# Performance work log

Hardware: AMD Instinct MI355X
Metric: run time of the kernel (lower is better)

Reference implementation:

```python
import jax, jax.numpy as jnp
import numpy as np

L, B, E = 2048, 4, 1024
H = 8
D1 = 2048          # expand_ratio * E, multiple of H
HD = D1 // H       # head dim 256
MAX_L = 2048
EPS = 1e-8


def setup_inputs() -> dict:
    key = jax.random.key(0)
    ks = jax.random.split(key, 9)
    std = 0.02
    return {
        "x": jax.random.normal(ks[0], (L, B, E), jnp.float32),
        "Wu": jax.random.normal(ks[1], (D1, E), jnp.float32) * std,
        "bu": jax.random.normal(ks[2], (D1,), jnp.float32) * std,
        "Wv": jax.random.normal(ks[3], (D1, E), jnp.float32) * std,
        "bv": jax.random.normal(ks[4], (D1,), jnp.float32) * std,
        "Wo": jax.random.normal(ks[5], (E, D1), jnp.float32) * std,
        "bo": jax.random.normal(ks[6], (E,), jnp.float32) * std,
        "zero": jax.random.normal(ks[7], (H, 1), jnp.float32) * 0.1,   # Toeplitz coef, offset 0
        "pos": jax.random.normal(ks[8], (H, MAX_L - 1), jnp.float32) * 0.1,  # offsets 1..n-1
    }


def _simple_rmsnorm(x):
    d = x.shape[-1]
    rms = jnp.linalg.norm(x, axis=-1, keepdims=True) * (d ** -0.5)
    return x / (rms + EPS)


def _toeplitz_causal_fft(v, zero, pos):
    # v: (b, h, n, hd); causal Toeplitz mixing along n via FFT long conv
    n = v.shape[-2]
    coef = jnp.concatenate([zero, pos[:, : n - 1]], axis=-1)  # (h, n)
    m = 2 * n
    cf = jnp.fft.rfft(coef, m, axis=-1)                  # (h, m//2+1)
    vf = jnp.fft.rfft(v, m, axis=-2)                     # (b, h, m//2+1, hd)
    out = jnp.fft.irfft(cf[None, :, :, None] * vf, m, axis=-2)
    return out[:, :, :n, :]


def reference(x, Wu, bu, Wv, bv, Wo, bo, zero, pos):
    # x: (n, b, e) fairseq layout
    n, b, e = x.shape
    shortcut = x
    xn = _simple_rmsnorm(x)                               # pre_norm (SimpleRMSNorm, no params)
    u = jax.nn.silu(jnp.einsum('nbe,de->nbd', xn, Wu) + bu)   # (n,b,d1)
    v = jax.nn.silu(jnp.einsum('nbe,de->nbd', xn, Wv) + bv)   # (n,b,d1)
    # 'n b (h d) -> b h n d'
    vh = v.transpose(1, 0, 2).reshape(b, n, H, HD).transpose(0, 2, 1, 3)
    oh = _toeplitz_causal_fft(vh, zero, pos)              # (b,h,n,hd)
    o = oh.transpose(0, 2, 1, 3).reshape(b, n, D1).transpose(1, 0, 2)  # (n,b,d1)
    o = u * o                                             # gating
    out = jnp.einsum('nbd,ed->nbe', o, Wo) + bo + shortcut
    return out
```

## Files before the change

kernel.cpp:

```cpp
#include <hip/hip_runtime.h>
#include <cstdint>
#include <cstddef>

#define LQ   2048
#define BQ   4
#define EQ   1024
#define HQ   8
#define D1Q  2048
#define HDQ  256
#define NBQ  (LQ*BQ)

typedef __bf16 bf16_t;
typedef __bf16 bf16x8 __attribute__((ext_vector_type(8)));
typedef __bf16 bf16x4 __attribute__((ext_vector_type(4)));
typedef float  f32x4  __attribute__((ext_vector_type(4)));

#define GAS1(p) ((const __attribute__((address_space(1))) void*)(p))
#define LAS3(p) ((__attribute__((address_space(3))) void*)(p))


__global__ __launch_bounds__(256) void convert_kernel(
    const float* __restrict__ Wu, const float* __restrict__ Wv,
    const float* __restrict__ Wo,
    bf16_t* __restrict__ Wub, bf16_t* __restrict__ Wvb,
    bf16_t* __restrict__ Wob)
{
    const size_t i = ((size_t)blockIdx.x * 256 + threadIdx.x) * 4;
    if (i < (size_t)D1Q * EQ) {
        float4 a = *(const float4*)(Wu + i);
        float4 b = *(const float4*)(Wv + i);
        float4 d = *(const float4*)(Wo + i);
        bf16x4 oa, ob, od;
        oa[0]=(bf16_t)a.x; oa[1]=(bf16_t)a.y; oa[2]=(bf16_t)a.z; oa[3]=(bf16_t)a.w;
        ob[0]=(bf16_t)b.x; ob[1]=(bf16_t)b.y; ob[2]=(bf16_t)b.z; ob[3]=(bf16_t)b.w;
        od[0]=(bf16_t)d.x; od[1]=(bf16_t)d.y; od[2]=(bf16_t)d.z; od[3]=(bf16_t)d.w;
        *(bf16x4*)(Wub + i) = oa;
        *(bf16x4*)(Wvb + i) = ob;
        *(bf16x4*)(Wob + i) = od;
    }
}

__global__ __launch_bounds__(256) void build_toep_tiles(
    const float* __restrict__ zero, const float* __restrict__ pos,
    bf16_t* __restrict__ Atiles)
{
    const int q = blockIdx.x;
    const int h = blockIdx.y;
    const int doff = (q - 3) * 32;
    const int tid = threadIdx.x;
    bf16_t* dst = Atiles + ((size_t)h * 64 + q) * (128 * 32);
    const int e0 = tid * 16;
    const int r = e0 >> 5;
    const int cbase = e0 & 31;
    bf16_t vals[16];
    #pragma unroll
    for (int j = 0; j < 16; ++j) {
        const int d = doff + r - (cbase + j);
        float v = 0.f;
        if (d == 0) v = zero[h];
        else if (d > 0) v = pos[(size_t)h * (LQ - 1) + d - 1];
        vals[j] = (bf16_t)v;
    }
    *(bf16x8*)(dst + e0)     = *(bf16x8*)(vals);
    *(bf16x8*)(dst + e0 + 8) = *(bf16x8*)(vals + 8);
}

__global__ __launch_bounds__(256) void rmsnorm_kernel(
    const float* __restrict__ x, bf16_t* __restrict__ xn)
{
    const int row = blockIdx.x;
    const int tid = threadIdx.x;
    const float4 v = ((const float4*)(x + (size_t)row * EQ))[tid];
    float ss = v.x*v.x + v.y*v.y + v.z*v.z + v.w*v.w;
    #pragma unroll
    for (int m = 32; m >= 1; m >>= 1) ss += __shfl_xor(ss, m, 64);
    __shared__ float red[4];
    const int wid = tid >> 6, lane = tid & 63;
    if (lane == 0) red[wid] = ss;
    __syncthreads();
    const float tot = red[0] + red[1] + red[2] + red[3];
    const float inv = 1.f / (sqrtf(tot * (1.f / EQ)) + 1e-8f);
    bf16x4 o;
    o[0] = (bf16_t)(v.x * inv); o[1] = (bf16_t)(v.y * inv);
    o[2] = (bf16_t)(v.z * inv); o[3] = (bf16_t)(v.w * inv);
    *(bf16x4*)(xn + (size_t)row * EQ + tid * 4) = o;
}


__global__ __launch_bounds__(512, 2) void gemm_uv(
    const bf16_t* __restrict__ A, const bf16_t* __restrict__ Bm,
    const float* __restrict__ bbu, const float* __restrict__ bbv,
    bf16_t* __restrict__ Ub, bf16_t* __restrict__ Vt)
{
    constexpr int K = EQ;
    constexpr int BUF = 24576;
    __shared__ alignas(16) char smem[3 * BUF];

    const int nwg   = gridDim.x * gridDim.y;
    const int bid0  = blockIdx.y * gridDim.x + blockIdx.x;
    const int chunkw = nwg >> 3;
    const int sb    = (bid0 & 7) * chunkw + (bid0 >> 3);
    const int bx    = sb % gridDim.x;
    const int by    = sb / gridDim.x;

    const int tid  = threadIdx.x;
    const int wid  = tid >> 6;
    const int lane = tid & 63;
    const int frow = lane & 15;
    const int c    = lane >> 4;
    const int m0 = by * 256;
    const int n0 = bx * 128;
    const int wm = wid >> 1, wn = wid & 1;
    const int wrm = wm * 64, wrn = wn * 64;

    const int g = (frow >> 1) & 3;
    const int offA0 = (wrm + frow) * 64 + ((c ^ g) << 4);
    const int offB0 = 16384 + (wrn + frow) * 64 + ((c ^ g) << 4);

    const int rA   = tid >> 2;
    const int soff = (((tid & 3) ^ ((rA >> 1) & 3)) << 4);
    const size_t lda2 = (size_t)K * 2;
    const char* sA = (const char*)A  + (size_t)(m0 + rA) * lda2 + soff;
    const char* sB = (const char*)Bm + (size_t)(n0 + rA) * lda2 + soff;

    auto STAGE = [&](int bf, int kt) {
        char* dA = smem + bf * BUF + wid * 1024;
        __builtin_amdgcn_global_load_lds(GAS1(sA + (size_t)kt * 64), LAS3(dA), 16, 0, 0);
        __builtin_amdgcn_global_load_lds(GAS1(sA + 128 * lda2 + (size_t)kt * 64),
                                         LAS3(dA + 8192), 16, 0, 0);
        char* dB = smem + bf * BUF + 16384 + wid * 1024;
        __builtin_amdgcn_global_load_lds(GAS1(sB + (size_t)kt * 64), LAS3(dB), 16, 0, 0);
    };

    f32x4 acc[4][4];
    #pragma unroll
    for (int i = 0; i < 4; ++i)
        #pragma unroll
        for (int j = 0; j < 4; ++j) acc[i][j] = (f32x4){0.f, 0.f, 0.f, 0.f};

    const int NT = K >> 5;

    STAGE(0, 0); STAGE(1, 1);
    asm volatile("s_waitcnt vmcnt(3)" ::: "memory");
    __builtin_amdgcn_s_barrier();

    int cur = 0, pb = 2;
    for (int t = 0; t < NT; ++t) {
        if (t + 2 < NT) STAGE(pb, t + 2);
        const char* base = smem + cur * BUF;
        bf16x8 av[4], bv[4];
        #pragma unroll
        for (int i = 0; i < 4; ++i) {
            av[i] = *(const bf16x8*)(base + offA0 + i * 1024);
            bv[i] = *(const bf16x8*)(base + offB0 + i * 1024);
        }
        __builtin_amdgcn_s_setprio(1);
        #pragma unroll
        for (int mi = 0; mi < 4; ++mi)
            #pragma unroll
            for (int ni = 0; ni < 4; ++ni)
                acc[mi][ni] = __builtin_amdgcn_mfma_f32_16x16x32_bf16(
                    av[mi], bv[ni], acc[mi][ni], 0, 0, 0);
        __builtin_amdgcn_s_setprio(0);
        if (t + 1 < NT) {
            if (t + 2 < NT) asm volatile("s_waitcnt vmcnt(3)" ::: "memory");
            else            asm volatile("s_waitcnt vmcnt(0)" ::: "memory");
            __builtin_amdgcn_s_barrier();
        }
        cur = (cur == 2) ? 0 : cur + 1;
        pb  = (pb  == 2) ? 0 : pb  + 1;
    }

    if (bx < 16) {
        const int fq = c * 4;
        #pragma unroll
        for (int mi = 0; mi < 4; ++mi) {
            #pragma unroll
            for (int ni = 0; ni < 4; ++ni) {
                const int gn = n0 + wrn + ni * 16 + frow;
                #pragma unroll
                for (int j = 0; j < 4; ++j) {
                    const int gm = m0 + wrm + mi * 16 + fq + j;
                    float v = acc[mi][ni][j] + bbu[gn];
                    v = v / (1.f + __expf(-v));
                    Ub[(size_t)gm * D1Q + gn] = (bf16_t)v;
                }
            }
        }
        return;
    }

    {
        const int n0v = n0 - 2048;
        const int hh  = n0v >> 8;
        const int hdb = (n0v & 255) + wrn;
        float bb[4];
        #pragma unroll
        for (int ni = 0; ni < 4; ++ni) bb[ni] = bbv[n0v + wrn + ni * 16 + frow];

        bf16_t* chunk = (bf16_t*)smem + wn * 8448;
        #pragma unroll
        for (int p = 0; p < 2; ++p) {
            __syncthreads();
            #pragma unroll
            for (int mi = 0; mi < 4; ++mi) {
                #pragma unroll
                for (int nio = 0; nio < 2; ++nio) {
                    const int ni = p * 2 + nio;
                    const int nl = nio * 16 + frow;
                    const int tl = wm * 16 + mi * 4 + c;
                    #pragma unroll
                    for (int j = 0; j < 4; ++j) {
                        float v = acc[mi][ni][j] + bb[ni];
                        v = v / (1.f + __expf(-v));
                        chunk[nl * 264 + j * 64 + tl] = (bf16_t)v;
                    }
                }
            }
            __syncthreads();
            const int nl    = lane & 31;
            const int thalf = lane >> 5;
            const int b2    = wm;
            const int hd    = hdb + p * 32 + nl;
            const int t0    = (m0 >> 2) + thalf * 32;
            const bf16_t* src = chunk + nl * 264 + b2 * 64 + thalf * 32;
            bf16_t* dst = Vt + (((size_t)hh * 4 + b2) * 256 + hd) * (size_t)LQ + t0;
            #pragma unroll
            for (int u = 0; u < 4; ++u)
                *(bf16x8*)(dst + u * 8) = *(const bf16x8*)(src + u * 8);
        }
    }
}

__global__ __launch_bounds__(512, 2) void gemm_toep(
    const bf16_t* __restrict__ VT, const bf16_t* __restrict__ Atiles,
    const bf16_t* __restrict__ U, bf16_t* __restrict__ O)
{
    constexpr int BUF = 24576;
    __shared__ alignas(16) char smem[3 * BUF];

    const int bid   = blockIdx.x;
    const int m_blk = 15 - (bid >> 5);
    const int sub   = bid & 31;
    const int h     = sub >> 2;
    const int n0    = (sub & 3) * 256;
    const int m0    = m_blk * 128;

    const int tid  = threadIdx.x;
    const int wid  = tid >> 6;
    const int lane = tid & 63;
    const int frow = lane & 15;
    const int c    = lane >> 4;
    const int wrm  = (wid >> 2) * 64;
    const int wrn  = (wid & 3) * 64;

    const int g = (frow >> 1) & 3;
    const int offA0 = (wrm + frow) * 64 + ((c ^ g) << 4);
    const int offB0 = 8192 + (wrn + frow) * 64 + ((c ^ g) << 4);

    const int rA   = tid >> 2;
    const int soff = (((tid & 3) ^ ((rA >> 1) & 3)) << 4);
    const char* Ah = (const char*)Atiles + (size_t)h * 64 * 8192;
    const size_t ldb = (size_t)LQ * 2;
    const char* sB = (const char*)VT + ((size_t)h * 1024 + n0 + rA) * ldb + soff;

    auto STAGE = [&](int bf, int kt) {
        const int q = 4 * m_blk + 3 - kt;
        const char* s = Ah + (size_t)q * 8192 + (size_t)rA * 64 + soff;
        __builtin_amdgcn_global_load_lds(GAS1(s),
                                         LAS3(smem + bf * BUF + wid * 1024), 16, 0, 0);
        char* dB = smem + bf * BUF + 8192 + wid * 1024;
        __builtin_amdgcn_global_load_lds(GAS1(sB + (size_t)kt * 64), LAS3(dB), 16, 0, 0);
        __builtin_amdgcn_global_load_lds(GAS1(sB + 128 * ldb + (size_t)kt * 64),
                                         LAS3(dB + 8192), 16, 0, 0);
    };

    f32x4 acc[4][4];
    #pragma unroll
    for (int i = 0; i < 4; ++i)
        #pragma unroll
        for (int j = 0; j < 4; ++j) acc[i][j] = (f32x4){0.f, 0.f, 0.f, 0.f};

    const int NT = 4 * m_blk + 4;

    STAGE(0, 0); STAGE(1, 1);
    asm volatile("s_waitcnt vmcnt(3)" ::: "memory");
    __builtin_amdgcn_s_barrier();

    int cur = 0, pb = 2;
    for (int t = 0; t < NT; ++t) {
        if (t + 2 < NT) STAGE(pb, t + 2);
        const char* base = smem + cur * BUF;
        bf16x8 av[4], bv[4];
        #pragma unroll
        for (int i = 0; i < 4; ++i) {
            av[i] = *(const bf16x8*)(base + offA0 + i * 1024);
            bv[i] = *(const bf16x8*)(base + offB0 + i * 1024);
        }
        __builtin_amdgcn_s_setprio(1);
        #pragma unroll
        for (int mi = 0; mi < 4; ++mi)
            #pragma unroll
            for (int ni = 0; ni < 4; ++ni)
                acc[mi][ni] = __builtin_amdgcn_mfma_f32_16x16x32_bf16(
                    av[mi], bv[ni], acc[mi][ni], 0, 0, 0);
        __builtin_amdgcn_s_setprio(0);
        if (t + 1 < NT) {
            if (t + 2 < NT) asm volatile("s_waitcnt vmcnt(3)" ::: "memory");
            else            asm volatile("s_waitcnt vmcnt(0)" ::: "memory");
            __builtin_amdgcn_s_barrier();
        }
        cur = (cur == 2) ? 0 : cur + 1;
        pb  = (pb  == 2) ? 0 : pb  + 1;
    }

    const int fq = c * 4;
    #pragma unroll
    for (int mi = 0; mi < 4; ++mi) {
        #pragma unroll
        for (int ni = 0; ni < 4; ++ni) {
            const int nn = n0 + wrn + ni * 16 + frow;
            const int b  = nn >> 8, hd = nn & 255;
            #pragma unroll
            for (int j = 0; j < 4; ++j) {
                const int t = m0 + wrm + mi * 16 + fq + j;
                const size_t idx = ((size_t)t * BQ + b) * D1Q + h * HDQ + hd;
                const float uval = (float)U[idx];
                O[idx] = (bf16_t)(uval * acc[mi][ni][j]);
            }
        }
    }
}

__global__ __launch_bounds__(512, 2) void gemm_fin(
    const bf16_t* __restrict__ A, const bf16_t* __restrict__ Bm,
    const float* __restrict__ bias, const float* __restrict__ res,
    float* __restrict__ Cf)
{
    constexpr int K = D1Q, N = EQ;
    constexpr int BUF = 24576;
    __shared__ alignas(16) char smem[3 * BUF];

    const int nwg   = gridDim.x * gridDim.y;
    const int bid0  = blockIdx.y * gridDim.x + blockIdx.x;
    const int chunkw = nwg >> 3;
    const int sb    = (bid0 & 7) * chunkw + (bid0 >> 3);
    const int bx    = sb % gridDim.x;
    const int by    = sb / gridDim.x;

    const int tid  = threadIdx.x;
    const int wid  = tid >> 6;
    const int lane = tid & 63;
    const int frow = lane & 15;
    const int c    = lane >> 4;
    const int m0 = by * 256;
    const int n0 = bx * 128;
    const int wm = wid >> 1, wn = wid & 1;
    const int wrm = wm * 64, wrn = wn * 64;

    const int g = (frow >> 1) & 3;
    const int offA0 = (wrm + frow) * 64 + ((c ^ g) << 4);
    const int offB0 = 16384 + (wrn + frow) * 64 + ((c ^ g) << 4);

    const int rA   = tid >> 2;
    const int soff = (((tid & 3) ^ ((rA >> 1) & 3)) << 4);
    const size_t lda2 = (size_t)K * 2;
    const char* sA = (const char*)A  + (size_t)(m0 + rA) * lda2 + soff;
    const char* sB = (const char*)Bm + (size_t)(n0 + rA) * lda2 + soff;

    auto STAGE = [&](int bf, int kt) {
        char* dA = smem + bf * BUF + wid * 1024;
        __builtin_amdgcn_global_load_lds(GAS1(sA + (size_t)kt * 64), LAS3(dA), 16, 0, 0);
        __builtin_amdgcn_global_load_lds(GAS1(sA + 128 * lda2 + (size_t)kt * 64),
                                         LAS3(dA + 8192), 16, 0, 0);
        char* dB = smem + bf * BUF + 16384 + wid * 1024;
        __builtin_amdgcn_global_load_lds(GAS1(sB + (size_t)kt * 64), LAS3(dB), 16, 0, 0);
    };

    f32x4 acc[4][4];
    #pragma unroll
    for (int i = 0; i < 4; ++i)
        #pragma unroll
        for (int j = 0; j < 4; ++j) acc[i][j] = (f32x4){0.f, 0.f, 0.f, 0.f};

    const int NT = K >> 5;

    STAGE(0, 0); STAGE(1, 1);
    asm volatile("s_waitcnt vmcnt(3)" ::: "memory");
    __builtin_amdgcn_s_barrier();

    int cur = 0, pb = 2;
    for (int t = 0; t < NT; ++t) {
        if (t + 2 < NT) STAGE(pb, t + 2);
        const char* base = smem + cur * BUF;
        bf16x8 av[4], bv[4];
        #pragma unroll
        for (int i = 0; i < 4; ++i) {
            av[i] = *(const bf16x8*)(base + offA0 + i * 1024);
            bv[i] = *(const bf16x8*)(base + offB0 + i * 1024);
        }
        __builtin_amdgcn_s_setprio(1);
        #pragma unroll
        for (int mi = 0; mi < 4; ++mi)
            #pragma unroll
            for (int ni = 0; ni < 4; ++ni)
                acc[mi][ni] = __builtin_amdgcn_mfma_f32_16x16x32_bf16(
                    av[mi], bv[ni], acc[mi][ni], 0, 0, 0);
        __builtin_amdgcn_s_setprio(0);
        if (t + 1 < NT) {
            if (t + 2 < NT) asm volatile("s_waitcnt vmcnt(3)" ::: "memory");
            else            asm volatile("s_waitcnt vmcnt(0)" ::: "memory");
            __builtin_amdgcn_s_barrier();
        }
        cur = (cur == 2) ? 0 : cur + 1;
        pb  = (pb  == 2) ? 0 : pb  + 1;
    }

    const int fq = c * 4;
    #pragma unroll
    for (int mi = 0; mi < 4; ++mi) {
        #pragma unroll
        for (int ni = 0; ni < 4; ++ni) {
            const int gn = n0 + wrn + ni * 16 + frow;
            #pragma unroll
            for (int j = 0; j < 4; ++j) {
                const int gm = m0 + wrm + mi * 16 + fq + j;
                Cf[(size_t)gm * N + gn] =
                    acc[mi][ni][j] + bias[gn] + res[(size_t)gm * N + gn];
            }
        }
    }
}


extern "C" void kernel_launch(void* const* d_in, const int* in_sizes, int n_in,
                              void* d_out, int out_size, void* d_ws, size_t ws_size,
                              hipStream_t stream)
{
    const float* x    = (const float*)d_in[0];
    const float* Wu   = (const float*)d_in[1];
    const float* bu   = (const float*)d_in[2];
    const float* Wv   = (const float*)d_in[3];
    const float* bv   = (const float*)d_in[4];
    const float* Wo   = (const float*)d_in[5];
    const float* bo   = (const float*)d_in[6];
    const float* zero = (const float*)d_in[7];
    const float* pos  = (const float*)d_in[8];
    float* out = (float*)d_out;

    char* ws = (char*)d_ws;
    size_t off = 0;
    auto alloc = [&](size_t bytes) {
        char* p = ws + off;
        off += (bytes + 255) & ~(size_t)255;
        return p;
    };
    bf16_t* xn     = (bf16_t*)alloc((size_t)NBQ * EQ * 2);
    bf16_t* Wub    = (bf16_t*)alloc((size_t)D1Q * EQ * 2);
    bf16_t* Wvb    = (bf16_t*)alloc((size_t)D1Q * EQ * 2);
    bf16_t* Wob    = (bf16_t*)alloc((size_t)EQ * D1Q * 2);
    bf16_t* Atiles = (bf16_t*)alloc((size_t)HQ * 64 * 4096 * 2);
    bf16_t* Ub     = (bf16_t*)alloc((size_t)NBQ * D1Q * 2);
    bf16_t* VTb    = (bf16_t*)alloc((size_t)NBQ * D1Q * 2);
    bf16_t* Ob     = (bf16_t*)alloc((size_t)NBQ * D1Q * 2);

    convert_kernel<<<2048, 256, 0, stream>>>(Wu, Wv, Wo, Wub, Wvb, Wob);
    build_toep_tiles<<<dim3(64, 8), 256, 0, stream>>>(zero, pos, Atiles);
    rmsnorm_kernel<<<NBQ, 256, 0, stream>>>(x, xn);

    dim3 g1(32, NBQ / 256);
    gemm_uv<<<g1, 512, 0, stream>>>(xn, Wub, bu, bv, Ub, VTb);

    gemm_toep<<<512, 512, 0, stream>>>(VTb, Atiles, Ub, Ob);

    dim3 g2(EQ / 128, NBQ / 256);
    gemm_fin<<<g2, 512, 0, stream>>>(Ob, Wob, bo, x, out);
}
```

Before: 198.4 us.

## Prepack weights in MFMA fragment order and load B directly into registers

Converts Wu/Wv/Wo into bf16 laid out in the per-lane MFMA fragment order, so the two projection GEMMs read the B operand straight from global memory into registers instead of staging it through LDS. The LDS buffers shrink to hold only the A operand, and the explicit vmcnt waits before each barrier are dropped. Correctness now depends on the compiler's own wait for the B loads also covering the earlier A prefetch. The output GEMM is retiled to 128x128 blocks of 256 threads with three blocks per CU requested. The trade-off is that per-iteration global B loads are not prefetched ahead, so their latency may be exposed, and the conversion kernel's reads are less coalesced.

```diff
diff --git a/kernel.cpp b/kernel.cpp
--- a/kernel.cpp
+++ b/kernel.cpp
@@ -19,24 +19,34 @@
 #define LAS3(p) ((__attribute__((address_space(3))) void*)(p))
 
 
-__global__ __launch_bounds__(256) void convert_kernel(
+__global__ __launch_bounds__(256) void convert_frag(
     const float* __restrict__ Wu, const float* __restrict__ Wv,
     const float* __restrict__ Wo,
-    bf16_t* __restrict__ Wub, bf16_t* __restrict__ Wvb,
-    bf16_t* __restrict__ Wob)
-{
-    const size_t i = ((size_t)blockIdx.x * 256 + threadIdx.x) * 4;
-    if (i < (size_t)D1Q * EQ) {
-        float4 a = *(const float4*)(Wu + i);
-        float4 b = *(const float4*)(Wv + i);
-        float4 d = *(const float4*)(Wo + i);
-        bf16x4 oa, ob, od;
-        oa[0]=(bf16_t)a.x; oa[1]=(bf16_t)a.y; oa[2]=(bf16_t)a.z; oa[3]=(bf16_t)a.w;
-        ob[0]=(bf16_t)b.x; ob[1]=(bf16_t)b.y; ob[2]=(bf16_t)b.z; ob[3]=(bf16_t)b.w;
-        od[0]=(bf16_t)d.x; od[1]=(bf16_t)d.y; od[2]=(bf16_t)d.z; od[3]=(bf16_t)d.w;
-        *(bf16x4*)(Wub + i) = oa;
-        *(bf16x4*)(Wvb + i) = ob;
-        *(bf16x4*)(Wob + i) = od;
+    bf16_t* __restrict__ Wuvf, bf16_t* __restrict__ Wof)
+{
+    const size_t T = (size_t)blockIdx.x * 256 + threadIdx.x;
+    if (T < 524288) {
+        const int chunk = (int)(T >> 6), lane = (int)(T & 63);
+        const int nb = chunk >> 5, kt = chunk & 31;
+        const int r  = nb * 16 + (lane & 15);
+        const int col = kt * 32 + (lane >> 4) * 8;
+        const float* src = (r < D1Q) ? Wu + (size_t)r * EQ + col
+                                     : Wv + (size_t)(r - D1Q) * EQ + col;
+        bf16x8 v;
+        #pragma unroll
+        for (int j = 0; j < 8; ++j) v[j] = (bf16_t)src[j];
+        *(bf16x8*)(Wuvf + T * 8) = v;
+    } else if (T < 524288 + 262144) {
+        const size_t T2 = T - 524288;
+        const int chunk = (int)(T2 >> 6), lane = (int)(T2 & 63);
+        const int nb = chunk >> 6, kt = chunk & 63;
+        const int r  = nb * 16 + (lane & 15);
+        const int col = kt * 32 + (lane >> 4) * 8;
+        const float* src = Wo + (size_t)r * D1Q + col;
+        bf16x8 v;
+        #pragma unroll
+        for (int j = 0; j < 8; ++j) v[j] = (bf16_t)src[j];
+        *(bf16x8*)(Wof + T2 * 8) = v;
     }
 }
 
@@ -88,12 +98,12 @@
 
 
 __global__ __launch_bounds__(512, 2) void gemm_uv(
-    const bf16_t* __restrict__ A, const bf16_t* __restrict__ Bm,
+    const bf16_t* __restrict__ A, const bf16_t* __restrict__ Bf,
     const float* __restrict__ bbu, const float* __restrict__ bbv,
     bf16_t* __restrict__ Ub, bf16_t* __restrict__ Vt)
 {
     constexpr int K = EQ;
-    constexpr int BUF = 24576;
+    constexpr int BUF = 16384;
     __shared__ alignas(16) char smem[3 * BUF];
 
     const int nwg   = gridDim.x * gridDim.y;
@@ -115,21 +125,23 @@
 
     const int g = (frow >> 1) & 3;
     const int offA0 = (wrm + frow) * 64 + ((c ^ g) << 4);
-    const int offB0 = 16384 + (wrn + frow) * 64 + ((c ^ g) << 4);
 
     const int rA   = tid >> 2;
     const int soff = (((tid & 3) ^ ((rA >> 1) & 3)) << 4);
     const size_t lda2 = (size_t)K * 2;
-    const char* sA = (const char*)A  + (size_t)(m0 + rA) * lda2 + soff;
-    const char* sB = (const char*)Bm + (size_t)(n0 + rA) * lda2 + soff;
+    const char* sA = (const char*)A + (size_t)(m0 + rA) * lda2 + soff;
+
+    const int nb0 = (n0 + wrn) >> 4;
+    const bf16_t* bp[4];
+    #pragma unroll
+    for (int ni = 0; ni < 4; ++ni)
+        bp[ni] = Bf + (((size_t)(nb0 + ni) * 32) * 64 + lane) * 8;
 
     auto STAGE = [&](int bf, int kt) {
         char* dA = smem + bf * BUF + wid * 1024;
         __builtin_amdgcn_global_load_lds(GAS1(sA + (size_t)kt * 64), LAS3(dA), 16, 0, 0);
         __builtin_amdgcn_global_load_lds(GAS1(sA + 128 * lda2 + (size_t)kt * 64),
                                          LAS3(dA + 8192), 16, 0, 0);
-        char* dB = smem + bf * BUF + 16384 + wid * 1024;
-        __builtin_amdgcn_global_load_lds(GAS1(sB + (size_t)kt * 64), LAS3(dB), 16, 0, 0);
     };
 
     f32x4 acc[4][4];
@@ -141,19 +153,21 @@
     const int NT = K >> 5;
 
     STAGE(0, 0); STAGE(1, 1);
-    asm volatile("s_waitcnt vmcnt(3)" ::: "memory");
+    asm volatile("s_waitcnt vmcnt(2)" ::: "memory");
     __builtin_amdgcn_s_barrier();
 
     int cur = 0, pb = 2;
     for (int t = 0; t < NT; ++t) {
+        bf16x8 bv[4];
+        #pragma unroll
+        for (int ni = 0; ni < 4; ++ni)
+            bv[ni] = *(const bf16x8*)(bp[ni] + (size_t)t * 512);
         if (t + 2 < NT) STAGE(pb, t + 2);
         const char* base = smem + cur * BUF;
-        bf16x8 av[4], bv[4];
-        #pragma unroll
-        for (int i = 0; i < 4; ++i) {
+        bf16x8 av[4];
+        #pragma unroll
+        for (int i = 0; i < 4; ++i)
             av[i] = *(const bf16x8*)(base + offA0 + i * 1024);
-            bv[i] = *(const bf16x8*)(base + offB0 + i * 1024);
-        }
         __builtin_amdgcn_s_setprio(1);
         #pragma unroll
         for (int mi = 0; mi < 4; ++mi)
@@ -162,11 +176,7 @@
                 acc[mi][ni] = __builtin_amdgcn_mfma_f32_16x16x32_bf16(
                     av[mi], bv[ni], acc[mi][ni], 0, 0, 0);
         __builtin_amdgcn_s_setprio(0);
-        if (t + 1 < NT) {
-            if (t + 2 < NT) asm volatile("s_waitcnt vmcnt(3)" ::: "memory");
-            else            asm volatile("s_waitcnt vmcnt(0)" ::: "memory");
-            __builtin_amdgcn_s_barrier();
-        }
+        if (t + 1 < NT) __builtin_amdgcn_s_barrier();
         cur = (cur == 2) ? 0 : cur + 1;
         pb  = (pb  == 2) ? 0 : pb  + 1;
     }
@@ -332,13 +342,13 @@
     }
 }
 
-__global__ __launch_bounds__(512, 2) void gemm_fin(
-    const bf16_t* __restrict__ A, const bf16_t* __restrict__ Bm,
+__global__ __launch_bounds__(256, 3) void gemm_fin(
+    const bf16_t* __restrict__ A, const bf16_t* __restrict__ Bf,
     const float* __restrict__ bias, const float* __restrict__ res,
     float* __restrict__ Cf)
 {
     constexpr int K = D1Q, N = EQ;
-    constexpr int BUF = 24576;
+    constexpr int BUF = 8192;
     __shared__ alignas(16) char smem[3 * BUF];
 
     const int nwg   = gridDim.x * gridDim.y;
@@ -353,28 +363,30 @@
     const int lane = tid & 63;
     const int frow = lane & 15;
     const int c    = lane >> 4;
-    const int m0 = by * 256;
+    const int m0 = by * 128;
     const int n0 = bx * 128;
     const int wm = wid >> 1, wn = wid & 1;
     const int wrm = wm * 64, wrn = wn * 64;
 
     const int g = (frow >> 1) & 3;
     const int offA0 = (wrm + frow) * 64 + ((c ^ g) << 4);
-    const int offB0 = 16384 + (wrn + frow) * 64 + ((c ^ g) << 4);
 
     const int rA   = tid >> 2;
     const int soff = (((tid & 3) ^ ((rA >> 1) & 3)) << 4);
     const size_t lda2 = (size_t)K * 2;
-    const char* sA = (const char*)A  + (size_t)(m0 + rA) * lda2 + soff;
-    const char* sB = (const char*)Bm + (size_t)(n0 + rA) * lda2 + soff;
+    const char* sA = (const char*)A + (size_t)(m0 + rA) * lda2 + soff;
+
+    const int nb0 = (n0 + wrn) >> 4;
+    const bf16_t* bp[4];
+    #pragma unroll
+    for (int ni = 0; ni < 4; ++ni)
+        bp[ni] = Bf + (((size_t)(nb0 + ni) * 64) * 64 + lane) * 8;
 
     auto STAGE = [&](int bf, int kt) {
         char* dA = smem + bf * BUF + wid * 1024;
         __builtin_amdgcn_global_load_lds(GAS1(sA + (size_t)kt * 64), LAS3(dA), 16, 0, 0);
-        __builtin_amdgcn_global_load_lds(GAS1(sA + 128 * lda2 + (size_t)kt * 64),
-                                         LAS3(dA + 8192), 16, 0, 0);
-        char* dB = smem + bf * BUF + 16384 + wid * 1024;
-        __builtin_amdgcn_global_load_lds(GAS1(sB + (size_t)kt * 64), LAS3(dB), 16, 0, 0);
+        __builtin_amdgcn_global_load_lds(GAS1(sA + 64 * lda2 + (size_t)kt * 64),
+                                         LAS3(dA + 4096), 16, 0, 0);
     };
 
     f32x4 acc[4][4];
@@ -386,19 +398,21 @@
     const int NT = K >> 5;
 
     STAGE(0, 0); STAGE(1, 1);
-    asm volatile("s_waitcnt vmcnt(3)" ::: "memory");
+    asm volatile("s_waitcnt vmcnt(2)" ::: "memory");
     __builtin_amdgcn_s_barrier();
 
     int cur = 0, pb = 2;
     for (int t = 0; t < NT; ++t) {
+        bf16x8 bv[4];
+        #pragma unroll
+        for (int ni = 0; ni < 4; ++ni)
+            bv[ni] = *(const bf16x8*)(bp[ni] + (size_t)t * 512);
         if (t + 2 < NT) STAGE(pb, t + 2);
         const char* base = smem + cur * BUF;
-        bf16x8 av[4], bv[4];
-        #pragma unroll
-        for (int i = 0; i < 4; ++i) {
+        bf16x8 av[4];
+        #pragma unroll
+        for (int i = 0; i < 4; ++i)
             av[i] = *(const bf16x8*)(base + offA0 + i * 1024);
-            bv[i] = *(const bf16x8*)(base + offB0 + i * 1024);
-        }
         __builtin_amdgcn_s_setprio(1);
         #pragma unroll
         for (int mi = 0; mi < 4; ++mi)
@@ -407,11 +421,7 @@
                 acc[mi][ni] = __builtin_amdgcn_mfma_f32_16x16x32_bf16(
                     av[mi], bv[ni], acc[mi][ni], 0, 0, 0);
         __builtin_amdgcn_s_setprio(0);
-        if (t + 1 < NT) {
-            if (t + 2 < NT) asm volatile("s_waitcnt vmcnt(3)" ::: "memory");
-            else            asm volatile("s_waitcnt vmcnt(0)" ::: "memory");
-            __builtin_amdgcn_s_barrier();
-        }
+        if (t + 1 < NT) __builtin_amdgcn_s_barrier();
         cur = (cur == 2) ? 0 : cur + 1;
         pb  = (pb  == 2) ? 0 : pb  + 1;
     }
@@ -456,23 +466,22 @@
         return p;
     };
     bf16_t* xn     = (bf16_t*)alloc((size_t)NBQ * EQ * 2);
-    bf16_t* Wub    = (bf16_t*)alloc((size_t)D1Q * EQ * 2);
-    bf16_t* Wvb    = (bf16_t*)alloc((size_t)D1Q * EQ * 2);
-    bf16_t* Wob    = (bf16_t*)alloc((size_t)EQ * D1Q * 2);
+    bf16_t* Wuvf   = (bf16_t*)alloc((size_t)4096 * EQ * 2);
+    bf16_t* Wof    = (bf16_t*)alloc((size_t)EQ * D1Q * 2);
     bf16_t* Atiles = (bf16_t*)alloc((size_t)HQ * 64 * 4096 * 2);
     bf16_t* Ub     = (bf16_t*)alloc((size_t)NBQ * D1Q * 2);
     bf16_t* VTb    = (bf16_t*)alloc((size_t)NBQ * D1Q * 2);
     bf16_t* Ob     = (bf16_t*)alloc((size_t)NBQ * D1Q * 2);
 
-    convert_kernel<<<2048, 256, 0, stream>>>(Wu, Wv, Wo, Wub, Wvb, Wob);
+    convert_frag<<<3072, 256, 0, stream>>>(Wu, Wv, Wo, Wuvf, Wof);
     build_toep_tiles<<<dim3(64, 8), 256, 0, stream>>>(zero, pos, Atiles);
     rmsnorm_kernel<<<NBQ, 256, 0, stream>>>(x, xn);
 
     dim3 g1(32, NBQ / 256);
-    gemm_uv<<<g1, 512, 0, stream>>>(xn, Wub, bu, bv, Ub, VTb);
+    gemm_uv<<<g1, 512, 0, stream>>>(xn, Wuvf, bu, bv, Ub, VTb);
 
     gemm_toep<<<512, 512, 0, stream>>>(VTb, Atiles, Ub, Ob);
 
-    dim3 g2(EQ / 128, NBQ / 256);
-    gemm_fin<<<g2, 512, 0, stream>>>(Ob, Wob, bo, x, out);
-}
+    dim3 g2(EQ / 128, NBQ / 128);
+    gemm_fin<<<g2, 256, 0, stream>>>(Ob, Wof, bo, x, out);
+}
```

After: 246.7 us. 24.4% more time.
